# Kernel tuning notes

Measured on AMD Instinct MI355X. Metric: run time of the kernel, lower is better.

## Reference

```python
import jax, jax.numpy as jnp
import numpy as np

B, D, HW, Z, PATCH = 16, 768, 32, 256, 16
N = HW * HW          # input_token_num = 1024
TOPK = N // 2        # topk=0.5 -> 512
EPS = 1e-5

def setup_inputs() -> dict:
    key = jax.random.key(0)
    ks = jax.random.split(key, 9)
    s = 0.02
    return {
        'image_features': jax.random.normal(ks[0], (B, D, HW, HW), jnp.float32),
        'w1': jax.random.normal(ks[1], (D, D), jnp.float32) * s,
        'b1': jnp.zeros((D,), jnp.float32),
        'w2': jax.random.normal(ks[2], (D, 1), jnp.float32) * s,
        'b2': jnp.zeros((1,), jnp.float32),
        'wp': jax.random.normal(ks[3], (D, Z), jnp.float32) * s,   # pre_projection
        'bp': jnp.zeros((Z,), jnp.float32),
        'mask_token': jnp.zeros((Z, 1), jnp.float32),              # init mode 0
        'conv_w': jax.random.normal(ks[4], (Z, Z), jnp.float32) * s,  # post_projection 1x1
        'conv_b': jnp.zeros((Z,), jnp.float32),
    }

def _upsample_nearest(m, f):
    # (B,1,h,w) -> (B,1,h*f,w*f)
    return jnp.repeat(jnp.repeat(m, f, axis=2), f, axis=3)

def reference(image_features, w1, b1, w2, b2, wp, bp, mask_token, conv_w, conv_b):
    x = image_features.transpose(0, 2, 3, 1).reshape(B, N, D)  # B (H W) C
    # score MLP: Linear-ReLU-Linear-Sigmoid
    h = jax.nn.relu(jnp.einsum('bnd,de->bne', x, w1) + b1)
    pred_score = jax.nn.sigmoid(jnp.einsum('bnd,de->bne', h, w2) + b2).reshape(B, N)
    score_sg = jax.lax.stop_gradient(pred_score)  # clone().detach()
    order = jnp.argsort(-score_sg, axis=1)        # descending sort
    top = order[:, :TOPK]                          # (B, K) int
    # LayerNorm (no affine) over channel dim
    mu = x.mean(-1, keepdims=True)
    var = x.var(-1, keepdims=True)
    xn = (x - mu) * jax.lax.rsqrt(var + EPS)
    # gather topk tokens, weight by (non-detached) score
    gathered = jnp.take_along_axis(xn, top[..., None], axis=1)
    gathered = gathered * jnp.take_along_axis(pred_score, top, axis=1)[..., None]
    sample_h = (jnp.einsum('bkd,dz->bkz', gathered, wp) + bp).transpose(0, 2, 1)  # B Z K
    # binary mask: scatter ones at topk positions
    mask = jnp.zeros((B, N), jnp.float32).at[jnp.arange(B)[:, None], top].set(1.0)
    binary_map = _upsample_nearest(mask.reshape(B, 1, HW, HW), PATCH)
    # normalized score map (global min/max over whole batch)
    smin, smax = score_sg.min(), score_sg.max()
    normed = (score_sg - smin) / jnp.maximum(smax - smin, EPS)
    score_map = _upsample_nearest(normed.reshape(B, 1, HW, HW), PATCH)
    # postforward: fill all N slots with mask_token, scatter sample_h at topk slots
    base = jnp.broadcast_to(mask_token, (Z, N))
    emb = jax.vmap(lambda hi, idx: base.at[:, idx].set(hi))(sample_h, top)  # (B,Z,N)
    emb = emb.reshape(B, Z, HW, HW)
    dec = jnp.einsum('oz,bzhw->bohw', conv_w, emb) + conv_b[None, :, None, None]
    return dec, binary_map, score_map
```

## Files before the change

### kernel.cpp

```cpp
#include <hip/hip_runtime.h>
#include <hip/hip_bf16.h>
#include <math.h>

#define B_ 16
#define D_ 768
#define N_ 1024
#define Z_ 256
#define TOPK_ 512
#define HW_ 32
#define EPS_ 1e-5f

typedef unsigned int uint;
typedef unsigned short ushort;
typedef __attribute__((ext_vector_type(4))) short short4v;
typedef __attribute__((ext_vector_type(8))) short bf16x8;
typedef __attribute__((ext_vector_type(4))) float f32x4;
typedef __attribute__((ext_vector_type(4))) int int4v;

__device__ __forceinline__ ushort f2bf(float v) {
  uint b = __float_as_uint(v);
  b += 0x7FFFu + ((b >> 16) & 1u);
  return (ushort)(b >> 16);
}
__device__ __forceinline__ float bf2f(ushort h) { return __uint_as_float(((uint)h) << 16); }
__device__ __forceinline__ int pk2(ushort a, ushort b) { return (int)((uint)a | ((uint)b << 16)); }

__global__ __launch_bounds__(256) void k_db(const float* __restrict__ cw,
                                            const float* __restrict__ cb,
                                            const float* __restrict__ bp,
                                            const float* __restrict__ mtk,
                                            float* __restrict__ db,
                                            float* __restrict__ bg) {
  __shared__ float s1[4], s2[4];
  int o = blockIdx.x, tid = threadIdx.x;
  float c = cw[o * Z_ + tid];
  float a1 = c * bp[tid], a2 = c * mtk[tid];
#pragma unroll
  for (int m = 32; m > 0; m >>= 1) { a1 += __shfl_xor(a1, m, 64); a2 += __shfl_xor(a2, m, 64); }
  if ((tid & 63) == 0) { s1[tid >> 6] = a1; s2[tid >> 6] = a2; }
  __syncthreads();
  if (tid == 0) {
    db[o] = cb[o] + s1[0] + s1[1] + s1[2] + s1[3];
    bg[o] = cb[o] + s2[0] + s2[1] + s2[2] + s2[3];
  }
}

__global__ __launch_bounds__(256) void k_cwT(const float* __restrict__ cw,
                                             float* __restrict__ cwT) {
  __shared__ float tile[32][33];
  int bx = blockIdx.x & 7, by = blockIdx.x >> 3;
  int tid = threadIdx.x;
#pragma unroll
  for (int it = 0; it < 4; ++it) {
    int idx = it * 256 + tid, r = idx >> 5, c = idx & 31;
    tile[r][c] = cw[(size_t)(by * 32 + r) * Z_ + bx * 32 + c];
  }
  __syncthreads();
#pragma unroll
  for (int it = 0; it < 4; ++it) {
    int idx = it * 256 + tid, r = idx >> 5, c = idx & 31;
    cwT[(size_t)(bx * 32 + r) * Z_ + by * 32 + c] = tile[c][r];
  }
}

__global__ __launch_bounds__(64) void k_w1pack(const float* __restrict__ w1,
                                               short* __restrict__ wA) {
  int lane = threadIdx.x;
  int f = blockIdx.x;
  int eg = f / 24, kkg = f % 24;
  int e = eg * 16 + (lane & 15);
  int d0 = kkg * 32 + 8 * (lane >> 4);
  ushort hh[8], ll[8];
#pragma unroll
  for (int j = 0; j < 8; ++j) {
    float v = w1[(size_t)(d0 + j) * D_ + e];
    hh[j] = f2bf(v);
    ll[j] = f2bf(v - bf2f(hh[j]));
  }
  int4v ph = {pk2(hh[0],hh[1]), pk2(hh[2],hh[3]), pk2(hh[4],hh[5]), pk2(hh[6],hh[7])};
  int4v pl = {pk2(ll[0],ll[1]), pk2(ll[2],ll[3]), pk2(ll[4],ll[5]), pk2(ll[6],ll[7])};
  int4v* W = (int4v*)wA;
  W[(size_t)f * 128 + lane] = ph;
  W[(size_t)f * 128 + 64 + lane] = pl;
}

__global__ __launch_bounds__(256) void k_mtpA(const float* __restrict__ wp,
                                              const float* __restrict__ cwT,
                                              short* __restrict__ mtA) {
  int o = threadIdx.x;
  int d0 = blockIdx.x * 8;
  int kkg = blockIdx.x >> 2, g = blockIdx.x & 3;
  float acc[8] = {0.f,0.f,0.f,0.f,0.f,0.f,0.f,0.f};
  for (int z = 0; z < Z_; ++z) {
    float c = cwT[(size_t)z * Z_ + o];
#pragma unroll
    for (int j = 0; j < 8; ++j) acc[j] += wp[(size_t)(d0 + j) * Z_ + z] * c;
  }
  int og = o >> 4, lane = (o & 15) + 16 * g;
  int4v p = {pk2(f2bf(acc[0]),f2bf(acc[1])), pk2(f2bf(acc[2]),f2bf(acc[3])),
             pk2(f2bf(acc[4]),f2bf(acc[5])), pk2(f2bf(acc[6]),f2bf(acc[7]))};
  ((int4v*)mtA)[(size_t)(og * 24 + kkg) * 64 + lane] = p;
}

__global__ __launch_bounds__(512, 2) void k_score_mfma(const float* __restrict__ xin,
                                                       const short* __restrict__ wA,
                                                       const float* __restrict__ b1,
                                                       const float* __restrict__ w2,
                                                       const float* __restrict__ b2,
                                                       float* __restrict__ score,
                                                       short* __restrict__ gtT) {
  __shared__ short panH[64 * 768];
  __shared__ short panL[64 * 128];
  __shared__ float redS[8][16][4], redQ[8][16][4];
  __shared__ float redL[8][4][16];
  __shared__ float ssc[64], ssh[64];
  int tid = threadIdx.x;
  int wave = tid >> 6, lane = tid & 63;
  int g = lane >> 4, cc = lane & 15;
  int b = blockIdx.x >> 4;
  int n0 = (blockIdx.x & 15) * 64;
  const float* xb = xin + (size_t)b * D_ * N_ + n0;
  int qt = tid & 15, qd = tid >> 4;
  int t0 = qt * 4, dl0 = qd * 4;
  float ss[4] = {0.f,0.f,0.f,0.f}, sq[4] = {0.f,0.f,0.f,0.f};
  f32x4 acc[6][4];
#pragma unroll
  for (int et = 0; et < 6; ++et)
#pragma unroll
    for (int tn = 0; tn < 4; ++tn) acc[et][tn] = (f32x4){0.f,0.f,0.f,0.f};
  const int4v* Ab = (const int4v*)wA;
  int eg0 = wave * 6;
  for (int kc = 0; kc < 6; ++kc) {
    float4 v0 = *(const float4*)(xb + (size_t)(kc*128 + dl0 + 0) * N_ + t0);
    float4 v1 = *(const float4*)(xb + (size_t)(kc*128 + dl0 + 1) * N_ + t0);
    float4 v2 = *(const float4*)(xb + (size_t)(kc*128 + dl0 + 2) * N_ + t0);
    float4 v3 = *(const float4*)(xb + (size_t)(kc*128 + dl0 + 3) * N_ + t0);
    ss[0] += v0.x+v1.x+v2.x+v3.x; sq[0] += v0.x*v0.x+v1.x*v1.x+v2.x*v2.x+v3.x*v3.x;
    ss[1] += v0.y+v1.y+v2.y+v3.y; sq[1] += v0.y*v0.y+v1.y*v1.y+v2.y*v2.y+v3.y*v3.y;
    ss[2] += v0.z+v1.z+v2.z+v3.z; sq[2] += v0.z*v0.z+v1.z*v1.z+v2.z*v2.z+v3.z*v3.z;
    ss[3] += v0.w+v1.w+v2.w+v3.w; sq[3] += v0.w*v0.w+v1.w*v1.w+v2.w*v2.w+v3.w*v3.w;
    __syncthreads();
#define STG(j, e0, e1, e2, e3) { \
    int t = t0 + (j); \
    int g1 = ((t & 7) ^ (t >> 3)); \
    int sbH = t * 768 + ((kc*128 + dl0) ^ (g1 << 3)); \
    int sbL = t * 128 + (dl0 ^ (g1 << 3)); \
    ushort h0 = f2bf(e0), h1 = f2bf(e1), h2 = f2bf(e2), h3 = f2bf(e3); \
    short4v ph = {(short)h0,(short)h1,(short)h2,(short)h3}; \
    short4v pl = {(short)f2bf((e0)-bf2f(h0)), (short)f2bf((e1)-bf2f(h1)), \
                  (short)f2bf((e2)-bf2f(h2)), (short)f2bf((e3)-bf2f(h3))}; \
    *(short4v*)&panH[sbH] = ph; \
    *(short4v*)&panL[sbL] = pl; }
    STG(0, v0.x, v1.x, v2.x, v3.x)
    STG(1, v0.y, v1.y, v2.y, v3.y)
    STG(2, v0.z, v1.z, v2.z, v3.z)
    STG(3, v0.w, v1.w, v2.w, v3.w)
#undef STG
    __syncthreads();
#pragma unroll
    for (int kk = 0; kk < 4; ++kk) {
      bf16x8 Bh[4], Bl[4];
#pragma unroll
      for (int tn = 0; tn < 4; ++tn) {
        int t = tn * 16 + cc;
        int g1 = ((t & 7) ^ (t >> 3));
        Bh[tn] = *(const bf16x8*)&panH[t * 768 + ((kc*128 + kk*32 + 8*g) ^ (g1 << 3))];
        Bl[tn] = *(const bf16x8*)&panL[t * 128 + ((kk*32 + 8*g) ^ (g1 << 3))];
      }
#pragma unroll
      for (int et = 0; et < 6; ++et) {
        size_t fidx = ((size_t)((eg0 + et) * 24 + (kc * 4 + kk))) * 128 + lane;
        union { int4v i; bf16x8 v; } ah, al;
        ah.i = Ab[fidx];
        al.i = Ab[fidx + 64];
#pragma unroll
        for (int tn = 0; tn < 4; ++tn) {
          acc[et][tn] = __builtin_amdgcn_mfma_f32_16x16x32_bf16(ah.v, Bh[tn], acc[et][tn], 0, 0, 0);
          acc[et][tn] = __builtin_amdgcn_mfma_f32_16x16x32_bf16(ah.v, Bl[tn], acc[et][tn], 0, 0, 0);
          acc[et][tn] = __builtin_amdgcn_mfma_f32_16x16x32_bf16(al.v, Bh[tn], acc[et][tn], 0, 0, 0);
        }
      }
    }
  }
#pragma unroll
  for (int j = 0; j < 4; ++j) {
    ss[j] += __shfl_xor(ss[j], 16, 64); sq[j] += __shfl_xor(sq[j], 16, 64);
    ss[j] += __shfl_xor(ss[j], 32, 64); sq[j] += __shfl_xor(sq[j], 32, 64);
  }
  if (lane < 16) {
#pragma unroll
    for (int j = 0; j < 4; ++j) { redS[wave][lane][j] = ss[j]; redQ[wave][lane][j] = sq[j]; }
  }
  float lg[4] = {0.f,0.f,0.f,0.f};
#pragma unroll
  for (int et = 0; et < 6; ++et) {
    int e = (eg0 + et) * 16 + 4 * g;
    float4 bb = *(const float4*)(b1 + e);
    float4 ww = *(const float4*)(w2 + e);
#pragma unroll
    for (int tn = 0; tn < 4; ++tn) {
      lg[tn] += fmaxf(acc[et][tn][0] + bb.x, 0.f) * ww.x;
      lg[tn] += fmaxf(acc[et][tn][1] + bb.y, 0.f) * ww.y;
      lg[tn] += fmaxf(acc[et][tn][2] + bb.z, 0.f) * ww.z;
      lg[tn] += fmaxf(acc[et][tn][3] + bb.w, 0.f) * ww.w;
    }
  }
#pragma unroll
  for (int tn = 0; tn < 4; ++tn) {
    lg[tn] += __shfl_xor(lg[tn], 16, 64);
    lg[tn] += __shfl_xor(lg[tn], 32, 64);
  }
  if (lane < 16) {
#pragma unroll
    for (int tn = 0; tn < 4; ++tn) redL[wave][tn][lane] = lg[tn];
  }
  __syncthreads();
  if (tid < 64) {
    int t = tid;
    float S = 0.f, Q = 0.f, L = 0.f;
#pragma unroll
    for (int w = 0; w < 8; ++w) {
      S += redS[w][t >> 2][t & 3];
      Q += redQ[w][t >> 2][t & 3];
      L += redL[w][t >> 4][t & 15];
    }
    float mu = S * (1.f / D_);
    float var = Q * (1.f / D_) - mu * mu;
    float rs = rsqrtf(var + EPS_);
    float sv = 1.f / (1.f + expf(-(L + b2[0])));
    score[b * N_ + n0 + t] = sv;
    float sc = rs * sv;
    ssc[t] = sc; ssh[t] = -mu * sc;
  }
  __syncthreads();
  {
    int t = tid >> 3, seg = tid & 7;
    int g1 = ((t & 7) ^ (t >> 3));
    float sc = ssc[t], sh = ssh[t];
    uint* gout = (uint*)(gtT + ((size_t)(b * N_ + n0 + t)) * D_ + seg * 96);
#pragma unroll
    for (int i = 0; i < 12; ++i) {
      int d8 = seg * 96 + i * 8;
      bf16x8 hv = *(const bf16x8*)&panH[t * 768 + (d8 ^ (g1 << 3))];
      uint u0 = pk2(f2bf(bf2f((ushort)hv[0])*sc+sh), f2bf(bf2f((ushort)hv[1])*sc+sh));
      uint u1 = pk2(f2bf(bf2f((ushort)hv[2])*sc+sh), f2bf(bf2f((ushort)hv[3])*sc+sh));
      uint u2 = pk2(f2bf(bf2f((ushort)hv[4])*sc+sh), f2bf(bf2f((ushort)hv[5])*sc+sh));
      uint u3 = pk2(f2bf(bf2f((ushort)hv[6])*sc+sh), f2bf(bf2f((ushort)hv[7])*sc+sh));
      int4v pv = {(int)u0, (int)u1, (int)u2, (int)u3};
      *(int4v*)(gout + i * 4) = pv;
    }
  }
}

__global__ __launch_bounds__(1024) void k_select(const float* __restrict__ score,
                                                 int* __restrict__ rank,
                                                 float* __restrict__ mm) {
  __shared__ float s[N_];
  __shared__ float red[32];
  int tid = threadIdx.x;
  int b = blockIdx.x >> 2;
  int tg = blockIdx.x & 3;
  s[tid] = score[b * N_ + tid];
  __syncthreads();
  int token = tg * 256 + (tid >> 2);
  int jq = tid & 3;
  float si = s[token];
  int cnt = 0;
  int j0 = jq * 256;
  for (int j = j0; j < j0 + 256; j += 4) {
    float4 sj = *reinterpret_cast<const float4*>(&s[j]);
    cnt += (sj.x > si) || (sj.x == si && (j + 0) < token);
    cnt += (sj.y > si) || (sj.y == si && (j + 1) < token);
    cnt += (sj.z > si) || (sj.z == si && (j + 2) < token);
    cnt += (sj.w > si) || (sj.w == si && (j + 3) < token);
  }
  cnt += __shfl_xor(cnt, 1, 64);
  cnt += __shfl_xor(cnt, 2, 64);
  if (jq == 0) rank[b * N_ + token] = cnt;
  if (tg == 0) {
    float v = s[tid];
    float mn = v, mx = v;
#pragma unroll
    for (int off = 32; off > 0; off >>= 1) {
      mn = fminf(mn, __shfl_xor(mn, off, 64));
      mx = fmaxf(mx, __shfl_xor(mx, off, 64));
    }
    if ((tid & 63) == 0) { red[tid >> 6] = mn; red[16 + (tid >> 6)] = mx; }
    __syncthreads();
    if (tid == 0) {
      float a = red[0], c = red[16];
      for (int w = 1; w < 16; ++w) { a = fminf(a, red[w]); c = fmaxf(c, red[16 + w]); }
      mm[2 * b] = a; mm[2 * b + 1] = c;
    }
  }
}

__global__ __launch_bounds__(256, 4) void k_gemm2dec(const short* __restrict__ gtT,
                                                     const short* __restrict__ mtA,
                                                     const float* __restrict__ db,
                                                     const float* __restrict__ bg,
                                                     const int* __restrict__ rank,
                                                     float* __restrict__ out) {
  __shared__ short pan[32 * 128];
  __shared__ int rks[32];
  int tid = threadIdx.x;
  int wave = tid >> 6, lane = tid & 63;
  int g = lane >> 4, cc = lane & 15;
  int bid = blockIdx.x;
  int b = bid >> 6, kt = (bid & 63) >> 1, oh = bid & 1;
  if (tid < 32) rks[tid] = rank[b * N_ + kt * 32 + tid];
  int srow = tid >> 3, scol = (tid & 7) * 16;
  const short* gb = gtT + (size_t)(b * N_ + kt * 32) * D_;
  f32x4 acc[2][2];
#pragma unroll
  for (int et = 0; et < 2; ++et)
#pragma unroll
    for (int tn = 0; tn < 2; ++tn) acc[et][tn] = (f32x4){0.f,0.f,0.f,0.f};
  const int4v* Am = (const int4v*)mtA;
  int sg1 = ((srow & 7) ^ (srow >> 3)) << 3;
  for (int kc = 0; kc < 6; ++kc) {
    int4v u0 = *(const int4v*)(gb + (size_t)srow * D_ + kc*128 + scol);
    int4v u1 = *(const int4v*)(gb + (size_t)srow * D_ + kc*128 + scol + 8);
    __syncthreads();
    *(int4v*)&pan[srow * 128 + (scol ^ sg1)] = u0;
    *(int4v*)&pan[srow * 128 + ((scol + 8) ^ sg1)] = u1;
    __syncthreads();
#pragma unroll
    for (int kk = 0; kk < 4; ++kk) {
      bf16x8 Bv[2];
#pragma unroll
      for (int tn = 0; tn < 2; ++tn) {
        int t = tn * 16 + cc;
        int g1 = ((t & 7) ^ (t >> 3));
        Bv[tn] = *(const bf16x8*)&pan[t * 128 + ((kk * 32 + 8 * g) ^ (g1 << 3))];
      }
#pragma unroll
      for (int et = 0; et < 2; ++et) {
        int og = oh * 8 + wave * 2 + et;
        size_t fidx = ((size_t)(og * 24 + (kc * 4 + kk))) * 64 + lane;
        union { int4v i; bf16x8 v; } av; av.i = Am[fidx];
#pragma unroll
        for (int tn = 0; tn < 2; ++tn)
          acc[et][tn] = __builtin_amdgcn_mfma_f32_16x16x32_bf16(av.v, Bv[tn], acc[et][tn], 0, 0, 0);
      }
    }
  }
  int rk0 = rks[cc], rk1 = rks[cc + 16];
#pragma unroll
  for (int et = 0; et < 2; ++et) {
    int og = oh * 8 + wave * 2 + et;
    int o0 = og * 16 + 4 * g;
#pragma unroll
    for (int r = 0; r < 4; ++r) {
      int o = o0 + r;
      float dbv = db[o], bgv = bg[o];
      float* orow = out + ((size_t)(b * Z_ + o)) * N_ + kt * 32 + cc;
      orow[0]  = (rk0 < TOPK_) ? acc[et][0][r] + dbv : bgv;
      orow[16] = (rk1 < TOPK_) ? acc[et][1][r] + dbv : bgv;
    }
  }
}

__global__ __launch_bounds__(128) void k_maps(const float* __restrict__ score,
                                              const int* __restrict__ rank,
                                              const float* __restrict__ mm,
                                              float* __restrict__ out) {
  int tid = threadIdx.x;
  int b = blockIdx.x >> 9;
  int ph = blockIdx.x & 511;
  float mn = mm[0], mx = mm[1];
#pragma unroll
  for (int w = 1; w < 16; ++w) { mn = fminf(mn, mm[2 * w]); mx = fmaxf(mx, mm[2 * w + 1]); }
  float inv = 1.f / fmaxf(mx - mn, EPS_);
  int pw0 = tid * 4;
  int cell = (ph >> 4) * HW_ + (pw0 >> 4);
  int rk = rank[b * N_ + cell];
  float bin = (rk < TOPK_) ? 1.f : 0.f;
  float sv = (score[b * N_ + cell] - mn) * inv;
  size_t base = (size_t)b * (512 * 512) + (size_t)ph * 512 + pw0;
  float4 bv = {bin, bin, bin, bin};
  float4 svv = {sv, sv, sv, sv};
  *reinterpret_cast<float4*>(out + 4194304 + base) = bv;
  *reinterpret_cast<float4*>(out + 8388608 + base) = svv;
}

extern "C" void kernel_launch(void* const* d_in, const int* in_sizes, int n_in,
                              void* d_out, int out_size, void* d_ws, size_t ws_size,
                              hipStream_t stream) {
  const float* xin = (const float*)d_in[0];
  const float* w1  = (const float*)d_in[1];
  const float* b1  = (const float*)d_in[2];
  const float* w2  = (const float*)d_in[3];
  const float* b2  = (const float*)d_in[4];
  const float* wp  = (const float*)d_in[5];
  const float* bp  = (const float*)d_in[6];
  const float* mtk = (const float*)d_in[7];
  const float* cw  = (const float*)d_in[8];
  const float* cb  = (const float*)d_in[9];
  float* out = (float*)d_out;

  short* wA    = (short*)d_ws;
  short* mtA   = wA + 1179648;
  short* gtT   = mtA + 196608;
  float* cwT   = (float*)(gtT + 12582912);
  float* db    = cwT + 65536;
  float* bg    = db + 256;
  float* score = bg + 256;
  float* mm    = score + 16384;
  int*   rank  = (int*)(mm + 32);

  k_db        <<<dim3(256),  dim3(256),  0, stream>>>(cw, cb, bp, mtk, db, bg);
  k_cwT       <<<dim3(64),   dim3(256),  0, stream>>>(cw, cwT);
  k_mtpA      <<<dim3(96),   dim3(256),  0, stream>>>(wp, cwT, mtA);
  k_w1pack    <<<dim3(1152), dim3(64),   0, stream>>>(w1, wA);
  k_score_mfma<<<dim3(256),  dim3(512),  0, stream>>>(xin, wA, b1, w2, b2, score, gtT);
  k_select    <<<dim3(64),   dim3(1024), 0, stream>>>(score, rank, mm);
  k_gemm2dec  <<<dim3(1024), dim3(256),  0, stream>>>(gtT, mtA, db, bg, rank, out);
  k_maps      <<<dim3(8192), dim3(128),  0, stream>>>(score, rank, mm, out);
}
```

Measured before the change: 222.1 us.

## Defer LayerNorm into second GEMM epilogue and double-buffer panel staging

New measurement: 230.7 us. +3.9%, slower.

```diff
diff --git a/kernel.cpp b/kernel.cpp
--- a/kernel.cpp
+++ b/kernel.cpp
@@ -25,23 +25,38 @@
 __device__ __forceinline__ float bf2f(ushort h) { return __uint_as_float(((uint)h) << 16); }
 __device__ __forceinline__ int pk2(ushort a, ushort b) { return (int)((uint)a | ((uint)b << 16)); }
 
+__global__ __launch_bounds__(256) void k_wsum(const float* __restrict__ wp,
+                                              float* __restrict__ wsum4) {
+  int z = threadIdx.x, h = blockIdx.x;
+  float s = 0.f;
+#pragma unroll 8
+  for (int d = h * 192; d < (h + 1) * 192; ++d) s += wp[(size_t)d * Z_ + z];
+  wsum4[h * Z_ + z] = s;
+}
+
 __global__ __launch_bounds__(256) void k_db(const float* __restrict__ cw,
                                             const float* __restrict__ cb,
                                             const float* __restrict__ bp,
                                             const float* __restrict__ mtk,
+                                            const float* __restrict__ wsum4,
                                             float* __restrict__ db,
-                                            float* __restrict__ bg) {
-  __shared__ float s1[4], s2[4];
+                                            float* __restrict__ bg,
+                                            float* __restrict__ M1) {
+  __shared__ float s1[4], s2[4], s3[4];
   int o = blockIdx.x, tid = threadIdx.x;
   float c = cw[o * Z_ + tid];
-  float a1 = c * bp[tid], a2 = c * mtk[tid];
-#pragma unroll
-  for (int m = 32; m > 0; m >>= 1) { a1 += __shfl_xor(a1, m, 64); a2 += __shfl_xor(a2, m, 64); }
-  if ((tid & 63) == 0) { s1[tid >> 6] = a1; s2[tid >> 6] = a2; }
+  float ws = wsum4[tid] + wsum4[Z_ + tid] + wsum4[2 * Z_ + tid] + wsum4[3 * Z_ + tid];
+  float a1 = c * bp[tid], a2 = c * mtk[tid], a3 = c * ws;
+#pragma unroll
+  for (int m = 32; m > 0; m >>= 1) {
+    a1 += __shfl_xor(a1, m, 64); a2 += __shfl_xor(a2, m, 64); a3 += __shfl_xor(a3, m, 64);
+  }
+  if ((tid & 63) == 0) { s1[tid >> 6] = a1; s2[tid >> 6] = a2; s3[tid >> 6] = a3; }
   __syncthreads();
   if (tid == 0) {
     db[o] = cb[o] + s1[0] + s1[1] + s1[2] + s1[3];
     bg[o] = cb[o] + s2[0] + s2[1] + s2[2] + s2[3];
+    M1[o] = s3[0] + s3[1] + s3[2] + s3[3];
   }
 }
 
@@ -91,6 +106,7 @@
   int d0 = blockIdx.x * 8;
   int kkg = blockIdx.x >> 2, g = blockIdx.x & 3;
   float acc[8] = {0.f,0.f,0.f,0.f,0.f,0.f,0.f,0.f};
+#pragma unroll 8
   for (int z = 0; z < Z_; ++z) {
     float c = cwT[(size_t)z * Z_ + o];
 #pragma unroll
@@ -108,12 +124,13 @@
                                                        const float* __restrict__ w2,
                                                        const float* __restrict__ b2,
                                                        float* __restrict__ score,
-                                                       short* __restrict__ gtT) {
-  __shared__ short panH[64 * 768];
-  __shared__ short panL[64 * 128];
+                                                       float* __restrict__ scv,
+                                                       float* __restrict__ shv,
+                                                       short* __restrict__ xbf) {
+  __shared__ short panH[2][64 * 128];
+  __shared__ short panL[2][64 * 128];
   __shared__ float redS[8][16][4], redQ[8][16][4];
   __shared__ float redL[8][4][16];
-  __shared__ float ssc[64], ssh[64];
   int tid = threadIdx.x;
   int wave = tid >> 6, lane = tid & 63;
   int g = lane >> 4, cc = lane & 15;
@@ -130,33 +147,36 @@
     for (int tn = 0; tn < 4; ++tn) acc[et][tn] = (f32x4){0.f,0.f,0.f,0.f};
   const int4v* Ab = (const int4v*)wA;
   int eg0 = wave * 6;
-  for (int kc = 0; kc < 6; ++kc) {
-    float4 v0 = *(const float4*)(xb + (size_t)(kc*128 + dl0 + 0) * N_ + t0);
-    float4 v1 = *(const float4*)(xb + (size_t)(kc*128 + dl0 + 1) * N_ + t0);
-    float4 v2 = *(const float4*)(xb + (size_t)(kc*128 + dl0 + 2) * N_ + t0);
-    float4 v3 = *(const float4*)(xb + (size_t)(kc*128 + dl0 + 3) * N_ + t0);
-    ss[0] += v0.x+v1.x+v2.x+v3.x; sq[0] += v0.x*v0.x+v1.x*v1.x+v2.x*v2.x+v3.x*v3.x;
-    ss[1] += v0.y+v1.y+v2.y+v3.y; sq[1] += v0.y*v0.y+v1.y*v1.y+v2.y*v2.y+v3.y*v3.y;
-    ss[2] += v0.z+v1.z+v2.z+v3.z; sq[2] += v0.z*v0.z+v1.z*v1.z+v2.z*v2.z+v3.z*v3.z;
-    ss[3] += v0.w+v1.w+v2.w+v3.w; sq[3] += v0.w*v0.w+v1.w*v1.w+v2.w*v2.w+v3.w*v3.w;
-    __syncthreads();
-#define STG(j, e0, e1, e2, e3) { \
+  float4 v0, v1, v2, v3;
+#define LOADC(kc) { \
+    v0 = *(const float4*)(xb + (size_t)((kc)*128 + dl0 + 0) * N_ + t0); \
+    v1 = *(const float4*)(xb + (size_t)((kc)*128 + dl0 + 1) * N_ + t0); \
+    v2 = *(const float4*)(xb + (size_t)((kc)*128 + dl0 + 2) * N_ + t0); \
+    v3 = *(const float4*)(xb + (size_t)((kc)*128 + dl0 + 3) * N_ + t0); }
+#define STG1(kc, bufsel, j, e0, e1, e2, e3) { \
     int t = t0 + (j); \
     int g1 = ((t & 7) ^ (t >> 3)); \
-    int sbH = t * 768 + ((kc*128 + dl0) ^ (g1 << 3)); \
-    int sbL = t * 128 + (dl0 ^ (g1 << 3)); \
+    int sb = t * 128 + (dl0 ^ (g1 << 3)); \
     ushort h0 = f2bf(e0), h1 = f2bf(e1), h2 = f2bf(e2), h3 = f2bf(e3); \
     short4v ph = {(short)h0,(short)h1,(short)h2,(short)h3}; \
     short4v pl = {(short)f2bf((e0)-bf2f(h0)), (short)f2bf((e1)-bf2f(h1)), \
                   (short)f2bf((e2)-bf2f(h2)), (short)f2bf((e3)-bf2f(h3))}; \
-    *(short4v*)&panH[sbH] = ph; \
-    *(short4v*)&panL[sbL] = pl; }
-    STG(0, v0.x, v1.x, v2.x, v3.x)
-    STG(1, v0.y, v1.y, v2.y, v3.y)
-    STG(2, v0.z, v1.z, v2.z, v3.z)
-    STG(3, v0.w, v1.w, v2.w, v3.w)
-#undef STG
-    __syncthreads();
+    *(short4v*)&panH[bufsel][sb] = ph; \
+    *(short4v*)&panL[bufsel][sb] = pl; \
+    *(short4v*)(xbf + ((size_t)(b * N_ + n0 + t)) * D_ + (kc)*128 + dl0) = ph; \
+    ss[j] += (e0)+(e1)+(e2)+(e3); \
+    sq[j] += (e0)*(e0)+(e1)*(e1)+(e2)*(e2)+(e3)*(e3); }
+#define STGC(kc, bufsel) { \
+    STG1(kc, bufsel, 0, v0.x, v1.x, v2.x, v3.x) \
+    STG1(kc, bufsel, 1, v0.y, v1.y, v2.y, v3.y) \
+    STG1(kc, bufsel, 2, v0.z, v1.z, v2.z, v3.z) \
+    STG1(kc, bufsel, 3, v0.w, v1.w, v2.w, v3.w) }
+  LOADC(0)
+  STGC(0, 0)
+  __syncthreads();
+  for (int kc = 0; kc < 6; ++kc) {
+    if (kc < 5) LOADC(kc + 1)
+    int bufsel = kc & 1;
 #pragma unroll
     for (int kk = 0; kk < 4; ++kk) {
       bf16x8 Bh[4], Bl[4];
@@ -164,8 +184,9 @@
       for (int tn = 0; tn < 4; ++tn) {
         int t = tn * 16 + cc;
         int g1 = ((t & 7) ^ (t >> 3));
-        Bh[tn] = *(const bf16x8*)&panH[t * 768 + ((kc*128 + kk*32 + 8*g) ^ (g1 << 3))];
-        Bl[tn] = *(const bf16x8*)&panL[t * 128 + ((kk*32 + 8*g) ^ (g1 << 3))];
+        int sb = t * 128 + ((kk * 32 + 8 * g) ^ (g1 << 3));
+        Bh[tn] = *(const bf16x8*)&panH[bufsel][sb];
+        Bl[tn] = *(const bf16x8*)&panL[bufsel][sb];
       }
 #pragma unroll
       for (int et = 0; et < 6; ++et) {
@@ -181,7 +202,14 @@
         }
       }
     }
-  }
+    if (kc < 5) {
+      STGC(kc + 1, bufsel ^ 1)
+      __syncthreads();
+    }
+  }
+#undef STGC
+#undef STG1
+#undef LOADC
 #pragma unroll
   for (int j = 0; j < 4; ++j) {
     ss[j] += __shfl_xor(ss[j], 16, 64); sq[j] += __shfl_xor(sq[j], 16, 64);
@@ -228,27 +256,11 @@
     float var = Q * (1.f / D_) - mu * mu;
     float rs = rsqrtf(var + EPS_);
     float sv = 1.f / (1.f + expf(-(L + b2[0])));
-    score[b * N_ + n0 + t] = sv;
+    int n = b * N_ + n0 + t;
     float sc = rs * sv;
-    ssc[t] = sc; ssh[t] = -mu * sc;
-  }
-  __syncthreads();
-  {
-    int t = tid >> 3, seg = tid & 7;
-    int g1 = ((t & 7) ^ (t >> 3));
-    float sc = ssc[t], sh = ssh[t];
-    uint* gout = (uint*)(gtT + ((size_t)(b * N_ + n0 + t)) * D_ + seg * 96);
-#pragma unroll
-    for (int i = 0; i < 12; ++i) {
-      int d8 = seg * 96 + i * 8;
-      bf16x8 hv = *(const bf16x8*)&panH[t * 768 + (d8 ^ (g1 << 3))];
-      uint u0 = pk2(f2bf(bf2f((ushort)hv[0])*sc+sh), f2bf(bf2f((ushort)hv[1])*sc+sh));
-      uint u1 = pk2(f2bf(bf2f((ushort)hv[2])*sc+sh), f2bf(bf2f((ushort)hv[3])*sc+sh));
-      uint u2 = pk2(f2bf(bf2f((ushort)hv[4])*sc+sh), f2bf(bf2f((ushort)hv[5])*sc+sh));
-      uint u3 = pk2(f2bf(bf2f((ushort)hv[6])*sc+sh), f2bf(bf2f((ushort)hv[7])*sc+sh));
-      int4v pv = {(int)u0, (int)u1, (int)u2, (int)u3};
-      *(int4v*)(gout + i * 4) = pv;
-    }
+    score[n] = sv;
+    scv[n] = sc;
+    shv[n] = -mu * sc;
   }
 }
 
@@ -295,68 +307,93 @@
   }
 }
 
-__global__ __launch_bounds__(256, 4) void k_gemm2dec(const short* __restrict__ gtT,
+__global__ __launch_bounds__(512, 2) void k_gemm2dec(const short* __restrict__ xbf,
                                                      const short* __restrict__ mtA,
                                                      const float* __restrict__ db,
                                                      const float* __restrict__ bg,
+                                                     const float* __restrict__ M1,
+                                                     const float* __restrict__ scv,
+                                                     const float* __restrict__ shv,
                                                      const int* __restrict__ rank,
                                                      float* __restrict__ out) {
-  __shared__ short pan[32 * 128];
-  __shared__ int rks[32];
+  __shared__ short pan[2][64 * 128];
+  __shared__ float lsc[64], lsh[64];
+  __shared__ int lrk[64];
   int tid = threadIdx.x;
   int wave = tid >> 6, lane = tid & 63;
   int g = lane >> 4, cc = lane & 15;
-  int bid = blockIdx.x;
-  int b = bid >> 6, kt = (bid & 63) >> 1, oh = bid & 1;
-  if (tid < 32) rks[tid] = rank[b * N_ + kt * 32 + tid];
+  int b = blockIdx.x >> 4;
+  int n0 = (blockIdx.x & 15) * 64;
+  if (tid < 64) {
+    int n = b * N_ + n0 + tid;
+    lsc[tid] = scv[n]; lsh[tid] = shv[n]; lrk[tid] = rank[n];
+  }
   int srow = tid >> 3, scol = (tid & 7) * 16;
-  const short* gb = gtT + (size_t)(b * N_ + kt * 32) * D_;
-  f32x4 acc[2][2];
+  int sg1 = ((srow & 7) ^ (srow >> 3)) << 3;
+  const short* gb = xbf + (size_t)(b * N_ + n0) * D_;
+  f32x4 acc[2][4];
 #pragma unroll
   for (int et = 0; et < 2; ++et)
 #pragma unroll
-    for (int tn = 0; tn < 2; ++tn) acc[et][tn] = (f32x4){0.f,0.f,0.f,0.f};
+    for (int tn = 0; tn < 4; ++tn) acc[et][tn] = (f32x4){0.f,0.f,0.f,0.f};
   const int4v* Am = (const int4v*)mtA;
-  int sg1 = ((srow & 7) ^ (srow >> 3)) << 3;
+  int4v u0, u1;
+#define GLOAD(kc) { \
+    u0 = *(const int4v*)(gb + (size_t)srow * D_ + (kc)*128 + scol); \
+    u1 = *(const int4v*)(gb + (size_t)srow * D_ + (kc)*128 + scol + 8); }
+#define PSTORE(bufsel) { \
+    *(int4v*)&pan[bufsel][srow * 128 + (scol ^ sg1)] = u0; \
+    *(int4v*)&pan[bufsel][srow * 128 + ((scol + 8) ^ sg1)] = u1; }
+  GLOAD(0)
+  PSTORE(0)
+  __syncthreads();
   for (int kc = 0; kc < 6; ++kc) {
-    int4v u0 = *(const int4v*)(gb + (size_t)srow * D_ + kc*128 + scol);
-    int4v u1 = *(const int4v*)(gb + (size_t)srow * D_ + kc*128 + scol + 8);
-    __syncthreads();
-    *(int4v*)&pan[srow * 128 + (scol ^ sg1)] = u0;
-    *(int4v*)&pan[srow * 128 + ((scol + 8) ^ sg1)] = u1;
-    __syncthreads();
+    if (kc < 5) GLOAD(kc + 1)
+    int bufsel = kc & 1;
 #pragma unroll
     for (int kk = 0; kk < 4; ++kk) {
-      bf16x8 Bv[2];
-#pragma unroll
-      for (int tn = 0; tn < 2; ++tn) {
+      bf16x8 Bv[4];
+#pragma unroll
+      for (int tn = 0; tn < 4; ++tn) {
         int t = tn * 16 + cc;
         int g1 = ((t & 7) ^ (t >> 3));
-        Bv[tn] = *(const bf16x8*)&pan[t * 128 + ((kk * 32 + 8 * g) ^ (g1 << 3))];
+        Bv[tn] = *(const bf16x8*)&pan[bufsel][t * 128 + ((kk * 32 + 8 * g) ^ (g1 << 3))];
       }
 #pragma unroll
       for (int et = 0; et < 2; ++et) {
-        int og = oh * 8 + wave * 2 + et;
+        int og = wave * 2 + et;
         size_t fidx = ((size_t)(og * 24 + (kc * 4 + kk))) * 64 + lane;
         union { int4v i; bf16x8 v; } av; av.i = Am[fidx];
 #pragma unroll
-        for (int tn = 0; tn < 2; ++tn)
+        for (int tn = 0; tn < 4; ++tn)
           acc[et][tn] = __builtin_amdgcn_mfma_f32_16x16x32_bf16(av.v, Bv[tn], acc[et][tn], 0, 0, 0);
       }
     }
-  }
-  int rk0 = rks[cc], rk1 = rks[cc + 16];
+    if (kc < 5) {
+      PSTORE(bufsel ^ 1)
+      __syncthreads();
+    }
+  }
+#undef GLOAD
+#undef PSTORE
 #pragma unroll
   for (int et = 0; et < 2; ++et) {
-    int og = oh * 8 + wave * 2 + et;
+    int og = wave * 2 + et;
     int o0 = og * 16 + 4 * g;
+    float4 dbv = *(const float4*)(db + o0);
+    float4 bgv = *(const float4*)(bg + o0);
+    float4 m1v = *(const float4*)(M1 + o0);
 #pragma unroll
     for (int r = 0; r < 4; ++r) {
       int o = o0 + r;
-      float dbv = db[o], bgv = bg[o];
-      float* orow = out + ((size_t)(b * Z_ + o)) * N_ + kt * 32 + cc;
-      orow[0]  = (rk0 < TOPK_) ? acc[et][0][r] + dbv : bgv;
-      orow[16] = (rk1 < TOPK_) ? acc[et][1][r] + dbv : bgv;
+      float dbr = ((const float*)&dbv)[r], bgr = ((const float*)&bgv)[r], m1r = ((const float*)&m1v)[r];
+      float* orow = out + ((size_t)(b * Z_ + o)) * N_ + n0 + cc;
+#pragma unroll
+      for (int tn = 0; tn < 4; ++tn) {
+        int tl = tn * 16 + cc;
+        float v = (lrk[tl] < TOPK_) ? lsc[tl] * acc[et][tn][r] + lsh[tl] * m1r + dbr : bgr;
+        orow[tn * 16] = v;
+      }
     }
   }
 }
@@ -401,20 +438,25 @@
 
   short* wA    = (short*)d_ws;
   short* mtA   = wA + 1179648;
-  short* gtT   = mtA + 196608;
-  float* cwT   = (float*)(gtT + 12582912);
-  float* db    = cwT + 65536;
+  short* xbf   = mtA + 196608;
+  float* cwT   = (float*)(xbf + 12582912);
+  float* wsum4 = cwT + 65536;
+  float* db    = wsum4 + 1024;
   float* bg    = db + 256;
-  float* score = bg + 256;
-  float* mm    = score + 16384;
+  float* M1    = bg + 256;
+  float* score = M1 + 256;
+  float* scv   = score + 16384;
+  float* shv   = scv + 16384;
+  float* mm    = shv + 16384;
   int*   rank  = (int*)(mm + 32);
 
-  k_db        <<<dim3(256),  dim3(256),  0, stream>>>(cw, cb, bp, mtk, db, bg);
+  k_wsum      <<<dim3(4),    dim3(256),  0, stream>>>(wp, wsum4);
+  k_db        <<<dim3(256),  dim3(256),  0, stream>>>(cw, cb, bp, mtk, wsum4, db, bg, M1);
   k_cwT       <<<dim3(64),   dim3(256),  0, stream>>>(cw, cwT);
   k_mtpA      <<<dim3(96),   dim3(256),  0, stream>>>(wp, cwT, mtA);
   k_w1pack    <<<dim3(1152), dim3(64),   0, stream>>>(w1, wA);
-  k_score_mfma<<<dim3(256),  dim3(512),  0, stream>>>(xin, wA, b1, w2, b2, score, gtT);
+  k_score_mfma<<<dim3(256),  dim3(512),  0, stream>>>(xin, wA, b1, w2, b2, score, scv, shv, xbf);
   k_select    <<<dim3(64),   dim3(1024), 0, stream>>>(score, rank, mm);
-  k_gemm2dec  <<<dim3(1024), dim3(256),  0, stream>>>(gtT, mtA, db, bg, rank, out);
+  k_gemm2dec  <<<dim3(256),  dim3(512),  0, stream>>>(xbf, mtA, db, bg, M1, scv, shv, rank, out);
   k_maps      <<<dim3(8192), dim3(128),  0, stream>>>(score, rank, mm, out);
 }
```
